# Optimization experiments

Measured on AMD Instinct MI355X. Metric: run time of the kernel, lower is better.

## Reference

```python
import jax, jax.numpy as jnp
import numpy as np
import math

# dims (match init_kwargs / input_specs)
T, B, S = 2048, 8, 512
D, H, DFF, NQ, W = 512, 8, 2048, 10, 16
EPS = 1e-5
NEG = -1e30


def _ln(x, g, b):
    mu = jnp.mean(x, axis=-1, keepdims=True)
    var = jnp.mean((x - mu) ** 2, axis=-1, keepdims=True)
    return (x - mu) * jax.lax.rsqrt(var + EPS) * g + b


def setup_inputs() -> dict:
    key = jax.random.key(0)
    ks = jax.random.split(key, 10)
    f = lambda k, shape, s=0.02: jax.random.normal(k, shape, jnp.float32) * s
    return {
        'tgt': jax.random.normal(ks[0], (T, B, D), jnp.float32),
        'memory': jax.random.normal(ks[1], (S, B, D), jnp.float32),
        'queries': f(ks[2], (NQ, D), 1.0 / math.sqrt(D)),
        'wk': f(ks[3], (NQ, 1), 1.0 / math.sqrt(NQ)),
        'in_proj_w': f(ks[4], (3 * D, D)),
        'in_proj_b': jnp.zeros((3 * D,), jnp.float32),
        'out_proj_w': f(ks[5], (D, D)),
        'out_proj_b': jnp.zeros((D,), jnp.float32),
        'lin1_w': f(ks[6], (DFF, D)),
        'lin1_b': jnp.zeros((DFF,), jnp.float32),
        'lin2_w': f(ks[7], (D, DFF)),
        'lin2_b': jnp.zeros((D,), jnp.float32),
        'ln1_g': jnp.ones((D,), jnp.float32), 'ln1_b': jnp.zeros((D,), jnp.float32),
        'ln2_g': jnp.ones((D,), jnp.float32), 'ln2_b': jnp.zeros((D,), jnp.float32),
        'ln3_g': jnp.ones((D,), jnp.float32), 'ln3_b': jnp.zeros((D,), jnp.float32),
    }


def _qa_block(x, queries, wk):
    # x: (T, B, D). Learned queries: per-head unit-norm + depth scale (QaN).
    dh = D // H
    q = queries.reshape(NQ, H, dh)
    q = q / (jnp.linalg.norm(q, axis=-1, keepdims=True) + 1e-6)
    q = (q / math.sqrt(dh)).reshape(NQ, D)
    # LocalAttention(window=W, look_backward=1, look_forward=1, non-causal, autopad)
    # k = v = x; T % W == 0 so autopad is a no-op.
    xb = jnp.transpose(x, (1, 0, 2))                       # (B, T, D)
    nw = T // W
    scale = D ** -0.5                                      # dim_head = D (single-head local attn)
    bk = xb.reshape(B, nw, W, D)
    pad = jnp.zeros((B, 1, W, D), x.dtype)
    bkp = jnp.concatenate([pad, bk, pad], axis=1)          # (B, nw+2, W, D)
    kv = jnp.concatenate([bkp[:, i:i + nw] for i in range(3)], axis=2)  # (B, nw, 3W, D)
    win_ok = jnp.pad(jnp.ones((nw,), bool), (1, 1))
    vm = jnp.stack([win_ok[i:i + nw] for i in range(3)], axis=1)        # (nw, 3)
    kmask = jnp.repeat(vm, W, axis=1)                                   # (nw, 3W)
    # The query vector is identical for every time step, so every position in a
    # window sees the same (query, keyset) pair -> one attention row per (n, window).
    sim = jnp.einsum('nd,bmjd->bnmj', q * scale, kv)       # (B, NQ, nw, 3W)
    sim = jnp.where(kmask[None, None], sim, NEG)
    attn = jax.nn.softmax(sim, axis=-1)
    out = jnp.einsum('bnmj,bmjd->bnmd', attn, kv)          # (B, NQ, nw, D)
    out = jnp.einsum('bnmd,n->bmd', out, wk[:, 0])         # mix N queries via wk (N,1)
    out = jnp.broadcast_to(out[:, :, None], (B, nw, W, D)).reshape(B, T, D)
    return jnp.transpose(out, (1, 0, 2))                   # (T, B, D)


def _mha_block(x, mem, in_w, in_b, out_w, out_b):
    dh = D // H
    wq, wkk, wv = jnp.split(in_w, 3, axis=0)
    bq, bk, bv = jnp.split(in_b, 3)
    q = (x @ wq.T + bq).reshape(T, B, H, dh).transpose(1, 2, 0, 3)   # (B,H,T,dh)
    k = (mem @ wkk.T + bk).reshape(S, B, H, dh).transpose(1, 2, 0, 3)
    v = (mem @ wv.T + bv).reshape(S, B, H, dh).transpose(1, 2, 0, 3)
    attn = jax.nn.softmax(jnp.einsum('bhtd,bhsd->bhts', q, k) / math.sqrt(dh), axis=-1)
    o = jnp.einsum('bhts,bhsd->bhtd', attn, v).transpose(2, 0, 1, 3).reshape(T, B, D)
    return o @ out_w.T + out_b


def reference(tgt, memory, queries, wk, in_proj_w, in_proj_b, out_proj_w, out_proj_b,
              lin1_w, lin1_b, lin2_w, lin2_b, ln1_g, ln1_b, ln2_g, ln2_b, ln3_g, ln3_b):
    # post-norm (norm_first=False), eval mode: dropouts + stochastic_depth(rate=0) are identity
    x = tgt
    x = _ln(x + _qa_block(x, queries, wk), ln1_g, ln1_b)
    x = _ln(x + _mha_block(x, memory, in_proj_w, in_proj_b, out_proj_w, out_proj_b), ln2_g, ln2_b)
    ff = jax.nn.relu(x @ lin1_w.T + lin1_b) @ lin2_w.T + lin2_b
    x = _ln(x + ff, ln3_g, ln3_b)
    # x = tgt + stochastic_depth(x - tgt) == x in eval / rate 0
    return x
```

## Files before the change

### kernel.cpp

```cpp
#include <hip/hip_runtime.h>


typedef unsigned short u16;
typedef unsigned int u32;
typedef short short8_t __attribute__((ext_vector_type(8)));
typedef float f32x4 __attribute__((ext_vector_type(4)));

#define TT 2048
#define BB 8
#define SS 512
#define DD 512
#define HH 8
#define DH 64
#define DFF 2048
#define NQ 10
#define WW 16
#define NW 128
#define KVPART 2097152

__device__ __forceinline__ float b2f(u16 u) {
    return __uint_as_float(((unsigned int)u) << 16);
}
__device__ __forceinline__ u16 f2b(float f) {
    unsigned int x = __float_as_uint(f);
    unsigned int r = x + 0x7FFFu + ((x >> 16) & 1u);
    return (u16)(r >> 16);
}
__device__ __forceinline__ u32 cvt_pk_bf16(float lo, float hi) {
    u32 r;
    asm volatile("v_cvt_pk_bf16_f32 %0, %1, %2" : "=v"(r) : "v"(lo), "v"(hi));
    return r;
}
__device__ __forceinline__ float wave_sum(float v) {
    #pragma unroll
    for (int o = 32; o > 0; o >>= 1) v += __shfl_xor(v, o, 64);
    return v;
}
__device__ __forceinline__ float wave_max(float v) {
    #pragma unroll
    for (int o = 32; o > 0; o >>= 1) v = fmaxf(v, __shfl_xor(v, o, 64));
    return v;
}
__device__ __forceinline__ void load4(const u16* p, float* v) {
    ushort4 t = *(const ushort4*)p;
    v[0] = b2f(t.x); v[1] = b2f(t.y); v[2] = b2f(t.z); v[3] = b2f(t.w);
}
__device__ __forceinline__ void load4(const float* p, float* v) {
    float4 t = *(const float4*)p;
    v[0] = t.x; v[1] = t.y; v[2] = t.z; v[3] = t.w;
}
__device__ __forceinline__ void st1(u16* p, float v) { *p = f2b(v); }
__device__ __forceinline__ void st1(float* p, float v) { *p = v; }

__device__ __forceinline__ void async16(const u16* g, u16* l) {
    __builtin_amdgcn_global_load_lds((const __attribute__((address_space(1))) u32*)g,
                                     (__attribute__((address_space(3))) u32*)l, 16, 0, 0);
}

__device__ __forceinline__ void xcd_remap(int& bx, int& by) {
    int flat = blockIdx.y * gridDim.x + blockIdx.x;
    int xcd = flat & 7;
    int j = flat >> 3;
    by = xcd * ((int)gridDim.y >> 3) + j / (int)gridDim.x;
    bx = j % (int)gridDim.x;
}

__device__ __forceinline__ void cvt_block(const float* s, u16* d, int base) {
    int i = base + threadIdx.x * 4;
    float4 v = *(const float4*)(s + i);
    ushort4 o;
    o.x = f2b(v.x); o.y = f2b(v.y); o.z = f2b(v.z); o.w = f2b(v.w);
    *(ushort4*)(d + i) = o;
}

__global__ __launch_bounds__(256) void cvt2_kernel(const float* __restrict__ s0,
                                                   const float* __restrict__ s1,
                                                   u16* __restrict__ d0,
                                                   u16* __restrict__ d1) {
    int bid = blockIdx.x;
    if (bid < 2048) cvt_block(s0, d0, bid * 1024);
    else            cvt_block(s1, d1, (bid - 2048) * 1024);
}

__global__ __launch_bounds__(256) void cvt3_kernel(const float* __restrict__ s0,
                                                   const float* __restrict__ s1,
                                                   const float* __restrict__ s2,
                                                   u16* __restrict__ d0,
                                                   u16* __restrict__ d1,
                                                   u16* __restrict__ d2) {
    int bid = blockIdx.x;
    if (bid < 256)       cvt_block(s0, d0, bid * 1024);
    else if (bid < 1280) cvt_block(s1, d1, (bid - 256) * 1024);
    else                 cvt_block(s2, d2, (bid - 1280) * 1024);
}

__global__ __launch_bounds__(512) void qeff_kernel(const float* __restrict__ queries,
                                                   float* __restrict__ qeff) {
    int d = threadIdx.x;
    const float KS = 0.0055242717280199026f;
    for (int n = 0; n < NQ; n++) {
        float v = queries[n * DD + d];
        float ss = wave_sum(v * v);
        float norm = sqrtf(ss);
        qeff[n * DD + d] = v / (norm + 1e-6f) * KS;
    }
}

__global__ __launch_bounds__(256) void p_kernel(const float* __restrict__ x,
                                                const float* __restrict__ qeff,
                                                float* __restrict__ p) {
    __shared__ float qe[NQ * DD];
    for (int i = threadIdx.x; i < NQ * DD; i += 256) qe[i] = qeff[i];
    __syncthreads();
    int b = blockIdx.x >> 9;
    int t = ((blockIdx.x & 511) << 2) + (threadIdx.x >> 6);
    int lane = threadIdx.x & 63;
    const float* xr = x + ((size_t)t * BB + b) * DD;
    float acc[NQ];
    #pragma unroll
    for (int n = 0; n < NQ; n++) acc[n] = 0.f;
    #pragma unroll
    for (int c = 0; c < 8; c++) {
        int d = c * 64 + lane;
        float xv = xr[d];
        #pragma unroll
        for (int n = 0; n < NQ; n++) acc[n] += xv * qe[n * DD + d];
    }
    #pragma unroll
    for (int n = 0; n < NQ; n++) {
        float s = wave_sum(acc[n]);
        if (lane == 0) p[((size_t)(b * NQ + n)) * TT + t] = s;
    }
}

__global__ __launch_bounds__(256) void winmix_kernel(const float* __restrict__ p,
                                                     const float* __restrict__ wk,
                                                     const float* __restrict__ x,
                                                     float* __restrict__ mixed) {
    __shared__ float As[48];
    int id = blockIdx.x;
    int b = id >> 7, m = id & 127;
    if (threadIdx.x < 64) {
        int j = threadIdx.x;
        int tj = (m - 1) * WW + j;
        bool valid = (j < 48) && (tj >= 0) && (tj < TT);
        float acc = 0.f;
        for (int n = 0; n < NQ; n++) {
            float v = valid ? p[((size_t)(b * NQ + n)) * TT + tj] : -1e30f;
            float mx = wave_max(v);
            float e = valid ? __expf(v - mx) : 0.f;
            float s = wave_sum(e);
            acc += wk[n] * (e / s);
        }
        if (j < 48) As[j] = acc;
    }
    __syncthreads();
    int d0 = threadIdx.x, d1 = threadIdx.x + 256;
    float a0 = 0.f, a1 = 0.f;
    int tb = (m - 1) * WW;
    for (int j = 0; j < 48; j++) {
        int t = tb + j;
        if ((unsigned)t < (unsigned)TT) {
            float aj = As[j];
            const float* xr = x + ((size_t)t * BB + b) * DD;
            a0 += aj * xr[d0];
            a1 += aj * xr[d1];
        }
    }
    mixed[(size_t)id * DD + d0] = a0;
    mixed[(size_t)id * DD + d1] = a1;
}

__global__ __launch_bounds__(256) void ln_qa_kernel(const float* __restrict__ a,
                                                    const float* __restrict__ mixed,
                                                    const float* __restrict__ g,
                                                    const float* __restrict__ bt,
                                                    u16* __restrict__ out) {
    int r = blockIdx.x * 4 + (threadIdx.x >> 6);
    int lane = threadIdx.x & 63;
    int t = r >> 3, b = r & 7;
    const float* ar = a + (size_t)r * DD;
    const float* mr = mixed + ((size_t)(b * NW + (t >> 4))) * DD;
    int d0 = lane * 8;
    float av[8], mv[8], gg[8], bb[8];
    load4(ar + d0, av); load4(ar + d0 + 4, av + 4);
    load4(mr + d0, mv); load4(mr + d0 + 4, mv + 4);
    load4(g + d0, gg);  load4(g + d0 + 4, gg + 4);
    load4(bt + d0, bb); load4(bt + d0 + 4, bb + 4);
    float v[8];
    float s = 0.f, s2 = 0.f;
    #pragma unroll
    for (int u = 0; u < 8; u++) { v[u] = av[u] + mv[u]; s += v[u]; s2 += v[u] * v[u]; }
    s = wave_sum(s); s2 = wave_sum(s2);
    float mu = s * (1.f / DD);
    float var = s2 * (1.f / DD) - mu * mu;
    float rs = rsqrtf(var + 1e-5f);
    #pragma unroll
    for (int u = 0; u < 8; u++) out[(size_t)r * DD + d0 + u] = f2b((v[u] - mu) * rs * gg[u] + bb[u]);
}

template <typename OT>
__global__ __launch_bounds__(256) void ln_rows_kernel(const u16* __restrict__ a,
                                                      const u16* __restrict__ bsrc,
                                                      const float* __restrict__ g,
                                                      const float* __restrict__ bt,
                                                      OT* __restrict__ out) {
    int r = blockIdx.x * 4 + (threadIdx.x >> 6);
    int lane = threadIdx.x & 63;
    const u16* ar = a + (size_t)r * DD;
    const u16* br = bsrc + (size_t)r * DD;
    int d0 = lane * 8;
    float av[8], cv[8], gg[8], bb[8];
    load4(ar + d0, av); load4(ar + d0 + 4, av + 4);
    load4(br + d0, cv); load4(br + d0 + 4, cv + 4);
    load4(g + d0, gg);  load4(g + d0 + 4, gg + 4);
    load4(bt + d0, bb); load4(bt + d0 + 4, bb + 4);
    float v[8];
    float s = 0.f, s2 = 0.f;
    #pragma unroll
    for (int u = 0; u < 8; u++) { v[u] = av[u] + cv[u]; s += v[u]; s2 += v[u] * v[u]; }
    s = wave_sum(s); s2 = wave_sum(s2);
    float mu = s * (1.f / DD);
    float var = s2 * (1.f / DD) - mu * mu;
    float rs = rsqrtf(var + 1e-5f);
    #pragma unroll
    for (int u = 0; u < 8; u++) st1(out + (size_t)r * DD + d0 + u, (v[u] - mu) * rs * gg[u] + bb[u]);
}

template <int RELU, int MT, int KV>
__global__ __launch_bounds__(256) void gemm_lds(const u16* __restrict__ A,
                                                const u16* __restrict__ W,
                                                const float* __restrict__ bias,
                                                u16* __restrict__ C,
                                                int M, int N, int K) {
    constexpr int BM = MT * 32;
    constexpr int NIA = BM / 64;
    __shared__ u16 As[2][BM * 32];
    __shared__ u16 Bs[2][128 * 32];
    int tid = threadIdx.x;
    int w = tid >> 6, lane = tid & 63;
    int n16 = lane & 15, quad = lane >> 4;
    int m0 = blockIdx.y * BM, n0 = blockIdx.x * 128;
    int wm16 = (w >> 1) * MT;
    int wn = (w & 1) * 64;

    const u16* gA[NIA];
    u16* lA[NIA];
    #pragma unroll
    for (int i = 0; i < NIA; i++) {
        int s = (w * NIA + i) * 64 + lane;
        int mb = s >> 6, kseg = (s >> 4) & 3, m = s & 15;
        gA[i] = A + (size_t)(m0 + mb * 16 + m) * K + kseg * 8;
        lA[i] = &As[0][(size_t)((w * NIA + i) * 64) * 8];
    }
    const u16* gB[2];
    u16* lB[2];
    #pragma unroll
    for (int i = 0; i < 2; i++) {
        int s = (w * 2 + i) * 64 + lane;
        int nb = s >> 6, kseg = (s >> 4) & 3, n = s & 15;
        gB[i] = W + (size_t)(n0 + nb * 16 + n) * K + kseg * 8;
        lB[i] = &Bs[0][(size_t)((w * 2 + i) * 64) * 8];
    }

    f32x4 acc[MT][4];
    #pragma unroll
    for (int i = 0; i < MT; i++)
        #pragma unroll
        for (int j = 0; j < 4; j++) acc[i][j] = (f32x4){0.f, 0.f, 0.f, 0.f};

    const int nk = K >> 5;
    #pragma unroll
    for (int i = 0; i < NIA; i++) async16(gA[i], lA[i]);
    #pragma unroll
    for (int i = 0; i < 2; i++) async16(gB[i], lB[i]);
    __syncthreads();

    for (int t = 0; t < nk; t++) {
        int cur = t & 1;
        if (t + 1 < nk) {
            int nxt = cur ^ 1;
            #pragma unroll
            for (int i = 0; i < NIA; i++) async16(gA[i] + (t + 1) * 32, lA[i] + nxt * (BM * 32));
            #pragma unroll
            for (int i = 0; i < 2; i++) async16(gB[i] + (t + 1) * 32, lB[i] + nxt * 4096);
        }
        const u16* Ac = &As[cur][0];
        const u16* Bc = &Bs[cur][0];
        short8_t af[MT], bf[4];
        #pragma unroll
        for (int im = 0; im < MT; im++)
            af[im] = *(const short8_t*)(Ac + (size_t)((wm16 + im) * 64 + lane) * 8);
        #pragma unroll
        for (int in = 0; in < 4; in++)
            bf[in] = *(const short8_t*)(Bc + (size_t)(((w & 1) * 4 + in) * 64 + lane) * 8);
        #pragma unroll
        for (int im = 0; im < MT; im++)
            #pragma unroll
            for (int in = 0; in < 4; in++)
                acc[im][in] = __builtin_amdgcn_mfma_f32_16x16x32_bf16(af[im], bf[in], acc[im][in], 0, 0, 0);
        __syncthreads();
    }

    float bia[4];
    #pragma unroll
    for (int in = 0; in < 4; in++) bia[in] = bias[n0 + wn + in * 16 + n16];
    #pragma unroll
    for (int im = 0; im < MT; im++) {
        #pragma unroll
        for (int r = 0; r < 4; r++) {
            int row = m0 + (wm16 + im) * 16 + quad * 4 + r;
            #pragma unroll
            for (int in = 0; in < 4; in++) {
                float v = acc[im][in][r] + bia[in];
                if (RELU) v = fmaxf(v, 0.f);
                if (KV) {
                    int col = n0 + wn + in * 16 + n16;
                    int part = col >> 9, h = (col >> 6) & 7, d = col & 63;
                    int s = row >> 3, bq = row & 7;
                    C[(size_t)part * KVPART + ((size_t)(bq * HH + h) * SS + s) * DH + d] = f2b(v);
                } else {
                    C[(size_t)row * N + n0 + wn + in * 16 + n16] = f2b(v);
                }
            }
        }
    }
}

template <int RELU, int KV>
__global__ __launch_bounds__(256) void gemm_np(const u16* __restrict__ A,
                                               const u16* __restrict__ W,
                                               const float* __restrict__ bias,
                                               u16* __restrict__ C,
                                               int M, int N, int K) {
    __shared__ u16 As[3][64 * 32];
    __shared__ u16 Bs[3][64 * 32];
    int tid = threadIdx.x;
    int w = tid >> 6, lane = tid & 63;
    int n16 = lane & 15, quad = lane >> 4;
    int bx, by;
    xcd_remap(bx, by);
    int m0 = by * 64, n0 = bx * 64;
    int wm16 = (w >> 1) * 2;
    int wn = (w & 1) * 32;

    const u16* gA0 = A + (size_t)(m0 + w * 16 + n16) * K + quad * 8;
    const u16* gB0 = W + (size_t)(n0 + w * 16 + n16) * K + quad * 8;

    f32x4 acc[2][2];
    #pragma unroll
    for (int i = 0; i < 2; i++)
        #pragma unroll
        for (int j = 0; j < 2; j++) acc[i][j] = (f32x4){0.f, 0.f, 0.f, 0.f};

    const int nk = K >> 5;
    async16(gA0, &As[0][w * 512]);
    async16(gB0, &Bs[0][w * 512]);
    async16(gA0 + 32, &As[1][w * 512]);
    async16(gB0 + 32, &Bs[1][w * 512]);

    int cur = 0;
    for (int t = 0; t < nk; t++) {
        if (t + 1 < nk) {
            __asm__ volatile("s_waitcnt vmcnt(2)" ::: "memory");
        } else {
            __asm__ volatile("s_waitcnt vmcnt(0)" ::: "memory");
        }
        __builtin_amdgcn_s_barrier();
        __builtin_amdgcn_sched_barrier(0);
        if (t + 2 < nk) {
            int nx2 = cur + 2; if (nx2 >= 3) nx2 -= 3;
            async16(gA0 + (t + 2) * 32, &As[nx2][w * 512]);
            async16(gB0 + (t + 2) * 32, &Bs[nx2][w * 512]);
        }
        const u16* Ac = &As[cur][0];
        const u16* Bc = &Bs[cur][0];
        short8_t af[2], bf[2];
        #pragma unroll
        for (int im = 0; im < 2; im++)
            af[im] = *(const short8_t*)(Ac + (size_t)((wm16 + im) * 64 + lane) * 8);
        #pragma unroll
        for (int in = 0; in < 2; in++)
            bf[in] = *(const short8_t*)(Bc + (size_t)(((w & 1) * 2 + in) * 64 + lane) * 8);
        #pragma unroll
        for (int im = 0; im < 2; im++)
            #pragma unroll
            for (int in = 0; in < 2; in++)
                acc[im][in] = __builtin_amdgcn_mfma_f32_16x16x32_bf16(af[im], bf[in], acc[im][in], 0, 0, 0);
        __asm__ volatile("s_waitcnt lgkmcnt(0)" ::: "memory");
        cur = (cur == 2) ? 0 : cur + 1;
    }

    float bia[2];
    #pragma unroll
    for (int in = 0; in < 2; in++) bia[in] = bias[n0 + wn + in * 16 + n16];
    #pragma unroll
    for (int im = 0; im < 2; im++) {
        #pragma unroll
        for (int r = 0; r < 4; r++) {
            int row = m0 + (wm16 + im) * 16 + quad * 4 + r;
            #pragma unroll
            for (int in = 0; in < 2; in++) {
                float v = acc[im][in][r] + bia[in];
                if (RELU) v = fmaxf(v, 0.f);
                if (KV) {
                    int col = n0 + wn + in * 16 + n16;
                    int part = col >> 9, h = (col >> 6) & 7, d = col & 63;
                    int s = row >> 3, bq = row & 7;
                    C[(size_t)part * KVPART + ((size_t)(bq * HH + h) * SS + s) * DH + d] = f2b(v);
                } else {
                    C[(size_t)row * N + n0 + wn + in * 16 + n16] = f2b(v);
                }
            }
        }
    }
}

__global__ __launch_bounds__(256) void attn_wp(const u16* __restrict__ qb,
                                               const u16* __restrict__ kvb,
                                               u16* __restrict__ ob) {
    __shared__ u16 Kb[2][2048];
    __shared__ u16 Vt[2][64][40];
    int tid = threadIdx.x;
    int w = tid >> 6, lane = tid & 63;
    int n16 = lane & 15, quad = lane >> 4, q8 = quad * 8;
    int xb, bh;
    xcd_remap(xb, bh);
    int b = bh >> 3, h = bh & 7;
    int q0 = xb * 128 + w * 32;

    short8_t aq[2][2];
    #pragma unroll
    for (int qt = 0; qt < 2; qt++) {
        const u16* qrow = qb + ((size_t)(q0 + qt * 16 + n16) * BB + b) * DD + h * DH;
        aq[qt][0] = *(const short8_t*)(qrow + q8);
        aq[qt][1] = *(const short8_t*)(qrow + 32 + q8);
    }

    const u16* kbase = kvb + (size_t)(b * HH + h) * (SS * DH);
    const u16* vbase = kvb + (size_t)KVPART + (size_t)(b * HH + h) * (SS * DH);

    const u16* gK = kbase + (size_t)((w >> 1) * 16 + n16) * DH + (w & 1) * 32 + q8;

    int m = lane & 15;
    int a2 = m >> 2, b2 = m & 3;
    int key0 = (b2 < 2) ? (4 * a2 + 2 * b2) : (16 + 4 * a2 + 2 * (b2 - 2));
    int kp2 = m * 2;
    int vd = w * 16 + quad * 4;
    const u16* gV = vbase + (size_t)key0 * DH + vd;

    float lsum[2] = {0.f, 0.f};
    f32x4 Oa[2][4];
    #pragma unroll
    for (int qt = 0; qt < 2; qt++)
        #pragma unroll
        for (int ot = 0; ot < 4; ot++) Oa[qt][ot] = (f32x4){0.f, 0.f, 0.f, 0.f};

    union VU { ushort4 q; u16 h[4]; };
    union PU { u32 wd[4]; short8_t s8; };

    {
        async16(gK, &Kb[0][w * 512]);
        VU va, vb2;
        va.q  = *(const ushort4*)(gV);
        vb2.q = *(const ushort4*)(gV + DH);
        #pragma unroll
        for (int u = 0; u < 4; u++)
            *(u32*)&Vt[0][vd + u][kp2] = (u32)va.h[u] | ((u32)vb2.h[u] << 16);
    }
    __syncthreads();

    for (int c = 0; c < 16; c++) {
        int cur = c & 1, nxt = cur ^ 1;

        VU va, vb2;
        if (c < 15) {
            const u16* gVc = gV + (size_t)(c + 1) * 32 * DH;
            va.q  = *(const ushort4*)(gVc);
            vb2.q = *(const ushort4*)(gVc + DH);
            async16(gK + (size_t)(c + 1) * 32 * DH, &Kb[nxt][w * 512]);
        }

        short8_t bk0 = *(const short8_t*)&Kb[cur][0 * 512 + lane * 8];
        short8_t bk1 = *(const short8_t*)&Kb[cur][1 * 512 + lane * 8];
        short8_t bk2 = *(const short8_t*)&Kb[cur][2 * 512 + lane * 8];
        short8_t bk3 = *(const short8_t*)&Kb[cur][3 * 512 + lane * 8];

        #pragma unroll
        for (int qt = 0; qt < 2; qt++) {
            f32x4 s0 = (f32x4){0.f, 0.f, 0.f, 0.f};
            s0 = __builtin_amdgcn_mfma_f32_16x16x32_bf16(bk0, aq[qt][0], s0, 0, 0, 0);
            s0 = __builtin_amdgcn_mfma_f32_16x16x32_bf16(bk1, aq[qt][1], s0, 0, 0, 0);
            f32x4 s1 = (f32x4){0.f, 0.f, 0.f, 0.f};
            s1 = __builtin_amdgcn_mfma_f32_16x16x32_bf16(bk2, aq[qt][0], s1, 0, 0, 0);
            s1 = __builtin_amdgcn_mfma_f32_16x16x32_bf16(bk3, aq[qt][1], s1, 0, 0, 0);

            float p0 = __expf(s0[0] * 0.125f - 8.0f);
            float p1 = __expf(s0[1] * 0.125f - 8.0f);
            float p2 = __expf(s0[2] * 0.125f - 8.0f);
            float p3 = __expf(s0[3] * 0.125f - 8.0f);
            float p4 = __expf(s1[0] * 0.125f - 8.0f);
            float p5 = __expf(s1[1] * 0.125f - 8.0f);
            float p6 = __expf(s1[2] * 0.125f - 8.0f);
            float p7 = __expf(s1[3] * 0.125f - 8.0f);
            lsum[qt] += ((p0 + p1) + (p2 + p3)) + ((p4 + p5) + (p6 + p7));

            PU pu;
            pu.wd[0] = cvt_pk_bf16(p0, p1);
            pu.wd[1] = cvt_pk_bf16(p2, p3);
            pu.wd[2] = cvt_pk_bf16(p4, p5);
            pu.wd[3] = cvt_pk_bf16(p6, p7);

            #pragma unroll
            for (int ot = 0; ot < 4; ot++) {
                short8_t bv = *(const short8_t*)&Vt[cur][ot * 16 + n16][q8];
                Oa[qt][ot] = __builtin_amdgcn_mfma_f32_16x16x32_bf16(pu.s8, bv, Oa[qt][ot], 0, 0, 0);
            }
        }

        if (c < 15) {
            #pragma unroll
            for (int u = 0; u < 4; u++)
                *(u32*)&Vt[nxt][vd + u][kp2] = (u32)va.h[u] | ((u32)vb2.h[u] << 16);
        }
        __syncthreads();
    }

    #pragma unroll
    for (int qt = 0; qt < 2; qt++) {
        float l = lsum[qt];
        l += __shfl_xor(l, 16, 64);
        l += __shfl_xor(l, 32, 64);
        #pragma unroll
        for (int r = 0; r < 4; r++) {
            float lq = __shfl(l, quad * 4 + r, 64);
            float inv = 1.f / lq;
            int t = q0 + qt * 16 + quad * 4 + r;
            u16* orow = ob + ((size_t)t * BB + b) * DD + h * DH + n16;
            #pragma unroll
            for (int ot = 0; ot < 4; ot++) orow[ot * 16] = f2b(Oa[qt][ot][r] * inv);
        }
    }
}

extern "C" void kernel_launch(void* const* d_in, const int* in_sizes, int n_in,
                              void* d_out, int out_size, void* d_ws, size_t ws_size,
                              hipStream_t stream) {
    const float* tgt       = (const float*)d_in[0];
    const float* memory    = (const float*)d_in[1];
    const float* queries   = (const float*)d_in[2];
    const float* wk        = (const float*)d_in[3];
    const float* in_proj_w = (const float*)d_in[4];
    const float* in_proj_b = (const float*)d_in[5];
    const float* out_proj_w= (const float*)d_in[6];
    const float* out_proj_b= (const float*)d_in[7];
    const float* lin1_w    = (const float*)d_in[8];
    const float* lin1_b    = (const float*)d_in[9];
    const float* lin2_w    = (const float*)d_in[10];
    const float* lin2_b    = (const float*)d_in[11];
    const float* ln1_g     = (const float*)d_in[12];
    const float* ln1_b     = (const float*)d_in[13];
    const float* ln2_g     = (const float*)d_in[14];
    const float* ln2_b     = (const float*)d_in[15];
    const float* ln3_g     = (const float*)d_in[16];
    const float* ln3_b     = (const float*)d_in[17];

    char* w = (char*)d_ws;
    float* qeff  = (float*)(w + 0);
    float* pbuf  = (float*)(w + 20480);
    float* mixed = (float*)(w + 872448);
    u16* y1  = (u16*)(w + 2969600);
    u16* qb  = (u16*)(w + 19746816);
    u16* kvb = (u16*)(w + 36524032);
    u16* ob  = (u16*)(w + 44912640);
    u16* ipwb = (u16*)(w + 44912640);
    u16* memb = (u16*)(w + 46485504);
    u16* opwb = (u16*)(w + 36524032);
    u16* l1wb = (u16*)(w + 37048320);
    u16* l2wb = (u16*)(w + 39145472);
    u16* t1 = qb;
    u16* y2 = ob;
    u16* hb = qb;
    u16* fb = y1;

    cvt2_kernel<<<2816, 256, 0, stream>>>(memory, in_proj_w, memb, ipwb);

    qeff_kernel<<<1, 512, 0, stream>>>(queries, qeff);
    p_kernel<<<BB * (TT / 4), 256, 0, stream>>>(tgt, qeff, pbuf);
    winmix_kernel<<<BB * NW, 256, 0, stream>>>(pbuf, wk, tgt, mixed);
    ln_qa_kernel<<<(TT * BB) / 4, 256, 0, stream>>>(tgt, mixed, ln1_g, ln1_b, y1);

    gemm_lds<0, 4, 0><<<dim3(DD / 128, (TT * BB) / 128), 256, 0, stream>>>(y1, ipwb, in_proj_b, qb, TT * BB, DD, DD);
    gemm_np<0, 1><<<dim3(1024 / 64, (SS * BB) / 64), 256, 0, stream>>>(memb, ipwb + (size_t)DD * DD, in_proj_b + DD, kvb, SS * BB, 1024, DD);
    attn_wp<<<dim3(TT / 128, BB * HH), 256, 0, stream>>>(qb, kvb, ob);
    cvt3_kernel<<<2304, 256, 0, stream>>>(out_proj_w, lin1_w, lin2_w, opwb, l1wb, l2wb);
    gemm_lds<0, 4, 0><<<dim3(DD / 128, (TT * BB) / 128), 256, 0, stream>>>(ob, opwb, out_proj_b, t1, TT * BB, DD, DD);
    ln_rows_kernel<u16><<<(TT * BB) / 4, 256, 0, stream>>>(y1, t1, ln2_g, ln2_b, y2);

    for (int c = 0; c < 4; c++) {
        const u16* y2c = y2 + (size_t)c * 4096 * DD;
        u16* fbc = fb + (size_t)c * 4096 * DD;
        gemm_lds<1, 4, 0><<<dim3(DFF / 128, 4096 / 128), 256, 0, stream>>>(y2c, l1wb, lin1_b, hb, 4096, DFF, DD);
        gemm_np<0, 0><<<dim3(DD / 64, 4096 / 64), 256, 0, stream>>>(hb, l2wb, lin2_b, fbc, 4096, DD, DFF);
    }
    ln_rows_kernel<float><<<(TT * BB) / 4, 256, 0, stream>>>(y2, fb, ln3_g, ln3_b, (float*)d_out);
}
```

Baseline: 526.3 us.

## Fuse FFN lin1+ReLU+lin2 into one kernel keeping hidden activations on-chip

```diff
diff --git a/kernel.cpp b/kernel.cpp
--- a/kernel.cpp
+++ b/kernel.cpp
@@ -412,6 +412,120 @@
                     C[(size_t)row * N + n0 + wn + in * 16 + n16] = f2b(v);
                 }
             }
+        }
+    }
+}
+
+__global__ __launch_bounds__(256, 1) void ffn_fused(const u16* __restrict__ A,
+                                                    const u16* __restrict__ W1,
+                                                    const float* __restrict__ b1,
+                                                    const u16* __restrict__ W2,
+                                                    const float* __restrict__ b2,
+                                                    u16* __restrict__ Cout) {
+    __shared__ u16 W1b[2][32 * 512];
+    __shared__ u16 Vt[2][512][40];
+    __shared__ float b1s[DFF];
+    int tid = threadIdx.x;
+    int w = tid >> 6, lane = tid & 63;
+    int n16 = lane & 15, quad = lane >> 4, q8 = quad * 8;
+    int m0 = blockIdx.x * 64;
+    int row = m0 + w * 16 + n16;
+
+    for (int i = tid; i < DFF; i += 256) b1s[i] = b1[i];
+
+    short8_t aq[16];
+    {
+        const u16* ar = A + (size_t)row * DD + q8;
+        #pragma unroll
+        for (int ks = 0; ks < 16; ks++)
+            aq[ks] = *(const short8_t*)(ar + ks * 32);
+    }
+
+    const u16* gW1 = W1 + (size_t)((w >> 1) * 16 + n16) * DD + ((w & 1) * 8) * 32 + q8;
+    int h4 = (tid & 7) * 4;
+    int pos = (h4 < 16) ? ((h4 >> 2) << 3) : ((((h4 - 16) >> 2) << 3) + 4);
+    const u16* gW2 = W2 + (size_t)(tid >> 3) * DFF + h4;
+
+    f32x4 acc[32];
+    #pragma unroll
+    for (int ot = 0; ot < 32; ot++) acc[ot] = (f32x4){0.f, 0.f, 0.f, 0.f};
+
+    union PU { u32 wd[4]; short8_t s8; };
+
+    #pragma unroll
+    for (int i = 0; i < 8; i++)
+        async16(gW1 + i * 32, &W1b[0][(size_t)(w * 8 + i) * 512]);
+    #pragma unroll
+    for (int i = 0; i < 16; i++) {
+        ushort4 v = *(const ushort4*)(gW2 + (size_t)i * 32 * DFF);
+        *(ushort4*)&Vt[0][i * 32 + (tid >> 3)][pos] = v;
+    }
+    __syncthreads();
+
+    for (int c = 0; c < 64; c++) {
+        int cur = c & 1, nxt = cur ^ 1;
+
+        ushort4 w2r[16];
+        if (c < 63) {
+            const u16* gW2c = gW2 + (size_t)(c + 1) * 32;
+            #pragma unroll
+            for (int i = 0; i < 16; i++)
+                w2r[i] = *(const ushort4*)(gW2c + (size_t)i * 32 * DFF);
+            const u16* gW1c = gW1 + (size_t)(c + 1) * 32 * DD;
+            #pragma unroll
+            for (int i = 0; i < 8; i++)
+                async16(gW1c + i * 32, &W1b[nxt][(size_t)(w * 8 + i) * 512]);
+        }
+
+        f32x4 s0 = (f32x4){0.f, 0.f, 0.f, 0.f};
+        f32x4 s1 = (f32x4){0.f, 0.f, 0.f, 0.f};
+        #pragma unroll
+        for (int ks = 0; ks < 16; ks++) {
+            short8_t f0 = *(const short8_t*)&W1b[cur][(size_t)ks * 512 + lane * 8];
+            s0 = __builtin_amdgcn_mfma_f32_16x16x32_bf16(f0, aq[ks], s0, 0, 0, 0);
+        }
+        #pragma unroll
+        for (int ks = 0; ks < 16; ks++) {
+            short8_t f1 = *(const short8_t*)&W1b[cur][(size_t)(16 + ks) * 512 + lane * 8];
+            s1 = __builtin_amdgcn_mfma_f32_16x16x32_bf16(f1, aq[ks], s1, 0, 0, 0);
+        }
+
+        float p0 = fmaxf(s0[0] + b1s[c * 32 + quad * 4 + 0], 0.f);
+        float p1 = fmaxf(s0[1] + b1s[c * 32 + quad * 4 + 1], 0.f);
+        float p2 = fmaxf(s0[2] + b1s[c * 32 + quad * 4 + 2], 0.f);
+        float p3 = fmaxf(s0[3] + b1s[c * 32 + quad * 4 + 3], 0.f);
+        float p4 = fmaxf(s1[0] + b1s[c * 32 + 16 + quad * 4 + 0], 0.f);
+        float p5 = fmaxf(s1[1] + b1s[c * 32 + 16 + quad * 4 + 1], 0.f);
+        float p6 = fmaxf(s1[2] + b1s[c * 32 + 16 + quad * 4 + 2], 0.f);
+        float p7 = fmaxf(s1[3] + b1s[c * 32 + 16 + quad * 4 + 3], 0.f);
+
+        PU pu;
+        pu.wd[0] = cvt_pk_bf16(p0, p1);
+        pu.wd[1] = cvt_pk_bf16(p2, p3);
+        pu.wd[2] = cvt_pk_bf16(p4, p5);
+        pu.wd[3] = cvt_pk_bf16(p6, p7);
+
+        #pragma unroll
+        for (int ot = 0; ot < 32; ot++) {
+            short8_t bv = *(const short8_t*)&Vt[cur][ot * 16 + n16][q8];
+            acc[ot] = __builtin_amdgcn_mfma_f32_16x16x32_bf16(pu.s8, bv, acc[ot], 0, 0, 0);
+        }
+
+        if (c < 63) {
+            #pragma unroll
+            for (int i = 0; i < 16; i++)
+                *(ushort4*)&Vt[nxt][i * 32 + (tid >> 3)][pos] = w2r[i];
+        }
+        __syncthreads();
+    }
+
+    #pragma unroll
+    for (int ot = 0; ot < 32; ot++) {
+        float bia = b2[ot * 16 + n16];
+        #pragma unroll
+        for (int r = 0; r < 4; r++) {
+            int ro = m0 + w * 16 + quad * 4 + r;
+            Cout[(size_t)ro * DD + ot * 16 + n16] = f2b(acc[ot][r] + bia);
         }
     }
 }
@@ -580,7 +694,6 @@
     u16* l2wb = (u16*)(w + 39145472);
     u16* t1 = qb;
     u16* y2 = ob;
-    u16* hb = qb;
     u16* fb = y1;
 
     cvt2_kernel<<<2816, 256, 0, stream>>>(memory, in_proj_w, memb, ipwb);
@@ -597,11 +710,6 @@
     gemm_lds<0, 4, 0><<<dim3(DD / 128, (TT * BB) / 128), 256, 0, stream>>>(ob, opwb, out_proj_b, t1, TT * BB, DD, DD);
     ln_rows_kernel<u16><<<(TT * BB) / 4, 256, 0, stream>>>(y1, t1, ln2_g, ln2_b, y2);
 
-    for (int c = 0; c < 4; c++) {
-        const u16* y2c = y2 + (size_t)c * 4096 * DD;
-        u16* fbc = fb + (size_t)c * 4096 * DD;
-        gemm_lds<1, 4, 0><<<dim3(DFF / 128, 4096 / 128), 256, 0, stream>>>(y2c, l1wb, lin1_b, hb, 4096, DFF, DD);
-        gemm_np<0, 0><<<dim3(DD / 64, 4096 / 64), 256, 0, stream>>>(hb, l2wb, lin2_b, fbc, 4096, DD, DFF);
-    }
+    ffn_fused<<<(TT * BB) / 64, 256, 0, stream>>>(y2, l1wb, lin1_b, l2wb, lin2_b, fb);
     ln_rows_kernel<float><<<(TT * BB) / 4, 256, 0, stream>>>(y2, fb, ln3_g, ln3_b, (float*)d_out);
 }
```

Result: faster. 472.8 us (-10.2%).
